# Kernel optimization log

Measured on AMD Instinct MI355X. Metric: run time of the kernel, lower is better.

Reference implementation:

```python
import jax, jax.numpy as jnp
import numpy as np

N_NODES = 100000


def gcn_conv(x, edge_index, W, b):
    # PyG GCNConv: add self-loops, symmetric normalization D^-1/2 (A+I) D^-1/2, then linear.
    n = x.shape[0]
    loop = jnp.arange(n, dtype=edge_index.dtype)
    src = jnp.concatenate([edge_index[0], loop])
    dst = jnp.concatenate([edge_index[1], loop])
    deg = jax.ops.segment_sum(jnp.ones_like(dst, dtype=x.dtype), dst, num_segments=n)
    dinv = jnp.where(deg > 0, jax.lax.rsqrt(deg), 0.0)
    norm = dinv[src] * dinv[dst]                      # [E+N]
    h = x @ W                                          # [N, out]
    msg = h[src] * norm[:, None]                       # gather + scale
    out = jax.ops.segment_sum(msg, dst, num_segments=n)  # scatter-add
    return out + b


def forward_one(x, edge_index, W1, b1, W2, b2, fc_w, fc_b):
    x = jax.nn.relu(gcn_conv(x, edge_index, W1, b1))
    x = jax.nn.relu(gcn_conv(x, edge_index, W2, b2))
    x = jnp.mean(x, axis=0)                            # [hidden]
    return x @ fc_w.T + fc_b


def setup_inputs() -> dict:
    key = jax.random.key(0)
    ks = jax.random.split(key, 10)
    d_in, d_h = 64, 64
    E = 1600000
    s = 1.0 / np.sqrt(d_in)
    return {
        "x1": jax.random.normal(ks[0], (N_NODES, d_in), jnp.float32),
        "x2": jax.random.normal(ks[1], (N_NODES, d_in), jnp.float32),
        "edge_index1": jax.random.randint(ks[2], (2, E), 0, N_NODES, jnp.int32),
        "edge_index2": jax.random.randint(ks[3], (2, E), 0, N_NODES, jnp.int32),
        "W1": jax.random.normal(ks[4], (d_in, d_h), jnp.float32) * s,
        "b1": jnp.zeros((d_h,), jnp.float32),
        "W2": jax.random.normal(ks[5], (d_h, d_h), jnp.float32) * s,
        "b2": jnp.zeros((d_h,), jnp.float32),
        "fc_w": jax.random.normal(ks[6], (d_h, d_h), jnp.float32) * s,
        "fc_b": jnp.zeros((d_h,), jnp.float32),
    }


def reference(x1, x2, edge_index1, edge_index2, W1, b1, W2, b2, fc_w, fc_b):
    out1 = forward_one(x1, edge_index1, W1, b1, W2, b2, fc_w, fc_b)
    out2 = forward_one(x2, edge_index2, W1, b1, W2, b2, fc_w, fc_b)
    return (out1, out2)
```

## Files before the change

kernel.cpp:

```cpp
#include <hip/hip_runtime.h>


#define TPB    256
#define CHUNK  128
#define SHIFT  7
#define KMAX   1024
#define CAP    2560
#define EPB    8192
#define CPAD   16

typedef __attribute__((ext_vector_type(8))) short short8;
typedef __attribute__((ext_vector_type(4))) float f32x4;
typedef __attribute__((ext_vector_type(2))) float float2v;

struct Ctx {
    const float* X; const int* esrc; const int* edst;
    unsigned int* temp; unsigned char* Hs2; unsigned char* Hs;
    unsigned int* csr; int* row_ptr; int* degA; float* dinv; int* cursorG;
    float* P; float* P2; float* outp;
};

__device__ __forceinline__ unsigned short f2bf(float x) {
    union { float f; unsigned int i; } c; c.f = x;
    unsigned int r = c.i + 0x7FFFu + ((c.i >> 16) & 1u);
    return (unsigned short)(r >> 16);
}
__device__ __forceinline__ unsigned char f2fp8(float x) {
    int p = __builtin_amdgcn_cvt_pk_fp8_f32(x, x, 0, false);
    return (unsigned char)(p & 0xFF);
}
__device__ __forceinline__ float2v up8lo(unsigned int w) {
    return __builtin_amdgcn_cvt_pk_f32_fp8(w, false);
}
__device__ __forceinline__ float2v up8hi(unsigned int w) {
    return __builtin_amdgcn_cvt_pk_f32_fp8(w, true);
}

__global__ void k_prepW2(const float* __restrict__ W1, const float* __restrict__ W2,
                         unsigned short* __restrict__ Wt1, unsigned short* __restrict__ Wt2) {
    const float* W = blockIdx.x ? W2 : W1;
    unsigned short* Wt = blockIdx.x ? Wt2 : Wt1;
    for (int i = threadIdx.x; i < 64 * 64; i += 256) {
        int n = i >> 6, k = i & 63;
        Wt[i] = f2bf(W[k * 64 + n]);
    }
}

__global__ void k_zeroCur(Ctx c0, Ctx c1, int nb0, int K, int N) {
    int b = blockIdx.x; Ctx c = c0;
    if (b >= nb0) { c = c1; b -= nb0; }
    int i = b * blockDim.x + threadIdx.x;
    if (i < K) c.cursorG[i * CPAD] = 0;
    if (b == 0 && threadIdx.x < 64) c.Hs[(size_t)N * 64 + threadIdx.x] = 0;
}

__global__ __launch_bounds__(1024) void k_binA(Ctx c0, Ctx c1, int nb0, int E, int K) {
    __shared__ int cnt[KMAX];
    __shared__ int ofs[KMAX];
    __shared__ int segBase[KMAX];
    __shared__ unsigned int sorted[EPB];
    __shared__ unsigned short bkt[EPB];
    int b = blockIdx.x; Ctx c = c0;
    if (b >= nb0) { c = c1; b -= nb0; }
    int tid = threadIdx.x;
    cnt[tid] = 0;
    __syncthreads();
    int base = b * EPB;
    int tot = E - base; if (tot > EPB) tot = EPB;
#pragma unroll
    for (int k = 0; k < EPB / 1024; ++k) {
        int e = base + k * 1024 + tid;
        if (e < E) atomicAdd(&cnt[c.edst[e] >> SHIFT], 1);
    }
    __syncthreads();
    int v = cnt[tid];
    segBase[tid] = v;
    __syncthreads();
#pragma unroll
    for (int off = 1; off < 1024; off <<= 1) {
        int t = (tid >= off) ? segBase[tid - off] : 0;
        __syncthreads();
        segBase[tid] += t;
        __syncthreads();
    }
    ofs[tid] = segBase[tid] - v;
    __syncthreads();
    if (tid < K) {
        segBase[tid] = v ? atomicAdd(&c.cursorG[tid * CPAD], v) : 0;
    } else {
        segBase[tid] = 0;
    }
    cnt[tid] = 0;
    __syncthreads();
#pragma unroll
    for (int k = 0; k < EPB / 1024; ++k) {
        int e = base + k * 1024 + tid;
        if (e < E) {
            int d = c.edst[e];
            int bk = d >> SHIFT;
            int r = atomicAdd(&cnt[bk], 1);
            int p = ofs[bk] + r;
            sorted[p] = ((unsigned int)(d & (CHUNK - 1)) << 17) | (unsigned int)c.esrc[e];
            bkt[p] = (unsigned short)bk;
        }
    }
    __syncthreads();
    for (int p = tid; p < tot; p += 1024) {
        unsigned int vv = sorted[p];
        int bk = bkt[p];
        int pos = segBase[bk] + (p - ofs[bk]);
        if (pos < CAP) c.temp[(size_t)bk * CAP + pos] = vv;
    }
}

__global__ __launch_bounds__(256) void k_csrb(Ctx c0, Ctx c1, int nb0, int N) {
    __shared__ int deg[CHUNK];
    __shared__ int lofs[CHUNK];
    __shared__ int cur[CHUNK];
    int b = blockIdx.x; Ctx c = c0;
    if (b >= nb0) { c = c1; b -= nb0; }
    int tid = threadIdx.x;
    if (tid < CHUNK) deg[tid] = 0;
    __syncthreads();
    int cnt = c.cursorG[b * CPAD]; if (cnt > CAP) cnt = CAP;
    const size_t tb = (size_t)b * CAP;
    for (int i = tid; i < cnt; i += 256) atomicAdd(&deg[c.temp[tb + i] >> 17], 1);
    __syncthreads();
    if (tid < CHUNK) lofs[tid] = deg[tid];
    __syncthreads();
#pragma unroll
    for (int off = 1; off < CHUNK; off <<= 1) {
        int t = (tid < CHUNK && tid >= off) ? lofs[tid - off] : 0;
        __syncthreads();
        if (tid < CHUNK) lofs[tid] += t;
        __syncthreads();
    }
    int base = b * CAP;
    if (tid < CHUNK) {
        int excl = lofs[tid] - deg[tid];
        lofs[tid] = excl;
        cur[tid] = 0;
        int node = b * CHUNK + tid;
        if (node < N) {
            c.row_ptr[node] = base + excl;
            c.degA[node] = deg[tid];
            c.dinv[node] = rsqrtf((float)deg[tid] + 1.0f);
        }
    }
    __syncthreads();
    for (int i = tid; i < cnt; i += 256) {
        unsigned int p = c.temp[tb + i];
        int dl = p >> 17;
        int rank = atomicAdd(&cur[dl], 1);
        c.csr[base + lofs[dl] + rank] = (p & 0x1FFFFu) << 6;
    }
}

__device__ __forceinline__ void mfma_tail(short8 a0, short8 a1,
                                          const unsigned short* __restrict__ Wt,
                                          unsigned char* __restrict__ Hs,
                                          int row0, int r, int q, int N) {
    short8 bfrag[4][2];
#pragma unroll
    for (int ct = 0; ct < 4; ++ct)
#pragma unroll
        for (int kb = 0; kb < 2; ++kb)
            bfrag[ct][kb] = *(const short8*)(Wt + (ct * 16 + r) * 64 + q * 8 + 32 * kb);
    f32x4 acc[4];
#pragma unroll
    for (int ct = 0; ct < 4; ++ct) {
        acc[ct] = (f32x4){0.0f, 0.0f, 0.0f, 0.0f};
        acc[ct] = __builtin_amdgcn_mfma_f32_16x16x32_bf16(a0, bfrag[ct][0], acc[ct], 0, 0, 0);
        acc[ct] = __builtin_amdgcn_mfma_f32_16x16x32_bf16(a1, bfrag[ct][1], acc[ct], 0, 0, 0);
    }
#pragma unroll
    for (int reg = 0; reg < 4; ++reg) {
        int row = row0 + q * 4 + reg;
        if (row < N) {
            size_t base = (size_t)row * 64 + r;
#pragma unroll
            for (int ct = 0; ct < 4; ++ct)
                Hs[base + ct * 16] = f2fp8(acc[ct][reg]);
        }
    }
}

__global__ __launch_bounds__(256) void k_gemm1(Ctx c0, Ctx c1, int nb0,
                                               const unsigned short* __restrict__ Wt,
                                               int nTiles, int N) {
    int b = blockIdx.x; Ctx c = c0;
    if (b >= nb0) { c = c1; b -= nb0; }
    int wave = threadIdx.x >> 6, lane = threadIdx.x & 63;
    int tile = b * 4 + wave;
    if (tile >= nTiles) return;
    int r = lane & 15, q = lane >> 4;
    int row0 = tile * 16;
    int row = row0 + r;
    int rr = row < N ? row : N - 1;
    float d = c.dinv[rr];
    const float* xrow = c.X + (size_t)rr * 64 + q * 8;
    short8 a0, a1;
#pragma unroll
    for (int j = 0; j < 8; ++j) a0[j] = (short)f2bf(xrow[j] * d);
#pragma unroll
    for (int j = 0; j < 8; ++j) a1[j] = (short)f2bf(xrow[32 + j] * d);
    mfma_tail(a0, a1, Wt, c.Hs, row0, r, q, N);
}

__device__ __forceinline__ void agg_map(int bi, int nb0, int swz,
                                        const Ctx& c0, const Ctx& c1,
                                        Ctx& c, int& b) {
    if (swz) {
        int graph = (bi >> 2) & 1;
        b = ((bi >> 3) << 2) | (bi & 3);
        c = graph ? c1 : c0;
    } else {
        b = bi; c = c0;
        if (b >= nb0) { c = c1; b -= nb0; }
    }
}

__device__ __forceinline__ void agg_issue8(const unsigned char* __restrict__ Hs,
                                           unsigned int idx, int slotbase, int lim,
                                           int hbase, int g, unsigned int s4,
                                           unsigned int* h) {
#pragma unroll
    for (int u = 0; u < 8; ++u) {
        if (slotbase + 2 * u >= lim) break;
        unsigned int su = (unsigned int)__shfl((int)idx, hbase + slotbase + 2 * u + g, 64);
        h[u] = *(const unsigned int*)(Hs + (su | s4));
    }
}
__device__ __forceinline__ void agg_cons8(const unsigned int* h, int slotbase, int lim,
                                          float2v* acc) {
#pragma unroll
    for (int u = 0; u < 8; ++u) {
        if (slotbase + 2 * u >= lim) break;
        acc[0] += up8lo(h[u]); acc[1] += up8hi(h[u]);
    }
}

__device__ __forceinline__ void agg_pair2(const unsigned char* __restrict__ Hs,
                                          const unsigned int* __restrict__ csr,
                                          int beg0, int deg0, int maxs0,
                                          int beg1, int deg1, int maxs1,
                                          int lane, unsigned int sent,
                                          float2v* acc0, float2v* acc1) {
    int hbase = lane & 32;
    int hl = lane & 31;
    int g = (lane >> 4) & 1;
    unsigned int s4 = (unsigned int)((lane & 15) * 4);
    unsigned int idx0 = (hl < deg0) ? csr[beg0 + hl] : sent;
    unsigned int idx1 = (hl < deg1) ? csr[beg1 + hl] : sent;
    int lim0 = maxs0 > 32 ? 32 : maxs0;
    int lim1 = maxs1 > 32 ? 32 : maxs1;
    unsigned int h0[8], h1[8];
    agg_issue8(Hs, idx0, 0, lim0, hbase, g, s4, h0);
    agg_issue8(Hs, idx1, 0, lim1, hbase, g, s4, h1);
    agg_cons8(h0, 0, lim0, acc0);
    if (lim0 > 16) agg_issue8(Hs, idx0, 16, lim0, hbase, g, s4, h0);
    agg_cons8(h1, 0, lim1, acc1);
    if (lim1 > 16) agg_issue8(Hs, idx1, 16, lim1, hbase, g, s4, h1);
    if (lim0 > 16) agg_cons8(h0, 16, lim0, acc0);
    if (lim1 > 16) agg_cons8(h1, 16, lim1, acc1);
    for (int base = 32; base < maxs0; base += 32) {
        unsigned int idx = (base + hl < deg0) ? csr[beg0 + base + hl] : sent;
        int lim = maxs0 - base; if (lim > 32) lim = 32;
        unsigned int hh[8];
        agg_issue8(Hs, idx, 0, lim, hbase, g, s4, hh);
        agg_cons8(hh, 0, lim, acc0);
        if (lim > 16) {
            agg_issue8(Hs, idx, 16, lim, hbase, g, s4, hh);
            agg_cons8(hh, 16, lim, acc0);
        }
    }
    for (int base = 32; base < maxs1; base += 32) {
        unsigned int idx = (base + hl < deg1) ? csr[beg1 + base + hl] : sent;
        int lim = maxs1 - base; if (lim > 32) lim = 32;
        unsigned int hh[8];
        agg_issue8(Hs, idx, 0, lim, hbase, g, s4, hh);
        agg_cons8(hh, 0, lim, acc1);
        if (lim > 16) {
            agg_issue8(Hs, idx, 16, lim, hbase, g, s4, hh);
            agg_cons8(hh, 16, lim, acc1);
        }
    }
#pragma unroll
    for (int k = 0; k < 2; ++k) {
        float2v o;
        o.x = __shfl_xor(acc0[k].x, 16, 64); o.y = __shfl_xor(acc0[k].y, 16, 64);
        acc0[k] += o;
        o.x = __shfl_xor(acc1[k].x, 16, 64); o.y = __shfl_xor(acc1[k].y, 16, 64);
        acc1[k] += o;
    }
}

__global__ __launch_bounds__(256) void k_agg1(Ctx c0, Ctx c1, int nb0, int swz,
                                              const float* __restrict__ bias,
                                              const unsigned short* __restrict__ Wt2,
                                              int n) {
    __shared__ unsigned short As[16][64];
    Ctx c; int b;
    agg_map(blockIdx.x, nb0, swz, c0, c1, c, b);
    int wave = threadIdx.x >> 6, lane = threadIdx.x & 63;
    int h = lane >> 5;
    int nbase = b * 16 + wave * 4;
    int node0 = nbase + h;
    int node1 = nbase + 2 + h;
    int nd0 = node0 < n ? node0 : 0;
    int nd1 = node1 < n ? node1 : 0;
    int beg0 = c.row_ptr[nd0];
    int beg1 = c.row_ptr[nd1];
    int deg0 = (node0 < n) ? c.degA[nd0] : 0;
    int deg1 = (node1 < n) ? c.degA[nd1] : 0;
    int od0 = __shfl_xor(deg0, 32, 64); int m0 = deg0 > od0 ? deg0 : od0;
    int od1 = __shfl_xor(deg1, 32, 64); int m1 = deg1 > od1 ? deg1 : od1;
    int maxs0 = __builtin_amdgcn_readfirstlane(m0);
    int maxs1 = __builtin_amdgcn_readfirstlane(m1);
    if (b == 0 && threadIdx.x < 64) c.Hs2[(size_t)n * 64 + threadIdx.x] = 0;
    float2v acc0[2] = {{0.f, 0.f}, {0.f, 0.f}};
    float2v acc1[2] = {{0.f, 0.f}, {0.f, 0.f}};
    agg_pair2(c.Hs, c.csr, beg0, deg0, maxs0, beg1, deg1, maxs1,
              lane, (unsigned int)n << 6, acc0, acc1);
    if (((lane >> 4) & 1) == 0) {
        int s = lane & 15;
#pragma unroll
        for (int pr = 0; pr < 2; ++pr) {
            const float2v* ac = pr ? acc1 : acc0;
            int node = nbase + pr * 2 + h;
            ushort4 o = {0, 0, 0, 0};
            if (node < n) {
                unsigned int hv = *(const unsigned int*)(c.Hs + (size_t)node * 64 + s * 4);
                float2v h0 = up8lo(hv), h1 = up8hi(hv);
                float4 bb = *(const float4*)(bias + s * 4);
                float d = c.dinv[node];
                o.x = f2bf(fmaxf(bb.x + d * (ac[0].x + h0.x), 0.0f) * d);
                o.y = f2bf(fmaxf(bb.y + d * (ac[0].y + h0.y), 0.0f) * d);
                o.z = f2bf(fmaxf(bb.z + d * (ac[1].x + h1.x), 0.0f) * d);
                o.w = f2bf(fmaxf(bb.w + d * (ac[1].y + h1.y), 0.0f) * d);
            }
            int row = wave * 4 + pr * 2 + h;
            *(ushort4*)(&As[row][(s * 4) ^ ((row & 7) << 3)]) = o;
        }
    }
    __syncthreads();
    {
        int r = lane & 15, q = lane >> 4;
        int sw = (r & 7) << 3;
        short8 a0 = *(const short8*)(&As[r][(q * 8) ^ sw]);
        short8 a1 = *(const short8*)(&As[r][(q * 8 + 32) ^ sw]);
        const unsigned short* wp = Wt2 + (wave * 16 + r) * 64 + q * 8;
        short8 b0 = *(const short8*)(wp);
        short8 b1 = *(const short8*)(wp + 32);
        f32x4 acc2 = {0.0f, 0.0f, 0.0f, 0.0f};
        acc2 = __builtin_amdgcn_mfma_f32_16x16x32_bf16(a0, b0, acc2, 0, 0, 0);
        acc2 = __builtin_amdgcn_mfma_f32_16x16x32_bf16(a1, b1, acc2, 0, 0, 0);
#pragma unroll
        for (int reg = 0; reg < 4; ++reg) {
            int l = q * 4 + reg;
            int row = b * 16 + l;
            if (row < n)
                c.Hs2[(size_t)row * 64 + wave * 16 + r] = f2fp8(acc2[reg]);
        }
    }
}

__global__ __launch_bounds__(256) void k_agg2(Ctx c0, Ctx c1, int nb0, int swz,
                                              const float* __restrict__ bias, int n) {
    __shared__ float red[16 * 64];
    Ctx c; int b;
    agg_map(blockIdx.x, nb0, swz, c0, c1, c, b);
    int wave = threadIdx.x >> 6, lane = threadIdx.x & 63;
    int h = lane >> 5;
    int nbase = b * 16 + wave * 4;
    int node0 = nbase + h;
    int node1 = nbase + 2 + h;
    int nd0 = node0 < n ? node0 : 0;
    int nd1 = node1 < n ? node1 : 0;
    int beg0 = c.row_ptr[nd0];
    int beg1 = c.row_ptr[nd1];
    int deg0 = (node0 < n) ? c.degA[nd0] : 0;
    int deg1 = (node1 < n) ? c.degA[nd1] : 0;
    int od0 = __shfl_xor(deg0, 32, 64); int m0 = deg0 > od0 ? deg0 : od0;
    int od1 = __shfl_xor(deg1, 32, 64); int m1 = deg1 > od1 ? deg1 : od1;
    int maxs0 = __builtin_amdgcn_readfirstlane(m0);
    int maxs1 = __builtin_amdgcn_readfirstlane(m1);
    float2v acc0[2] = {{0.f, 0.f}, {0.f, 0.f}};
    float2v acc1[2] = {{0.f, 0.f}, {0.f, 0.f}};
    agg_pair2(c.Hs2, c.csr, beg0, deg0, maxs0, beg1, deg1, maxs1,
              lane, (unsigned int)n << 6, acc0, acc1);
    if (((lane >> 4) & 1) == 0) {
        int s = lane & 15;
#pragma unroll
        for (int pr = 0; pr < 2; ++pr) {
            const float2v* ac = pr ? acc1 : acc0;
            int node = nbase + pr * 2 + h;
            float4 v = {0.f, 0.f, 0.f, 0.f};
            if (node < n) {
                unsigned int hv = *(const unsigned int*)(c.Hs2 + (size_t)node * 64 + s * 4);
                float2v h0 = up8lo(hv), h1 = up8hi(hv);
                float4 bb = *(const float4*)(bias + s * 4);
                float d = c.dinv[node];
                v.x = fmaxf(bb.x + d * (ac[0].x + h0.x), 0.0f);
                v.y = fmaxf(bb.y + d * (ac[0].y + h0.y), 0.0f);
                v.z = fmaxf(bb.z + d * (ac[1].x + h1.x), 0.0f);
                v.w = fmaxf(bb.w + d * (ac[1].y + h1.y), 0.0f);
            }
            *(float4*)(&red[(wave * 4 + pr * 2 + h) * 64 + s * 4]) = v;
        }
    }
    __syncthreads();
    if (threadIdx.x < 64) {
        float acc16 = 0.0f;
#pragma unroll
        for (int r = 0; r < 16; ++r) acc16 += red[r * 64 + threadIdx.x];
        c.P[(size_t)b * 64 + threadIdx.x] = acc16;
    }
}

__global__ void k_colsum(Ctx c0, Ctx c1, int nb0, int rows) {
    int b = blockIdx.x; Ctx c = c0;
    if (b >= nb0) { c = c1; b -= nb0; }
    int f = threadIdx.x;
    float acc = 0.0f;
    for (int r = b; r < rows; r += nb0) acc += c.P[(size_t)r * 64 + f];
    c.P2[b * 64 + f] = acc;
}

__global__ void k_fc(Ctx c0, Ctx c1, const float* __restrict__ fcw,
                     const float* __restrict__ fcb, int n) {
    Ctx c = blockIdx.x ? c1 : c0;
    __shared__ float S[64];
    int j = threadIdx.x;
    float s = 0.0f;
    for (int r = 0; r < 256; ++r) s += c.P2[r * 64 + j];
    S[j] = s;
    __syncthreads();
    float inv = 1.0f / (float)n;
    float acc = fcb[j];
#pragma unroll
    for (int k = 0; k < 64; ++k) acc += (S[k] * inv) * fcw[j * 64 + k];
    c.outp[j] = acc;
}

extern "C" void kernel_launch(void* const* d_in, const int* in_sizes, int n_in,
                              void* d_out, int out_size, void* d_ws, size_t ws_size,
                              hipStream_t stream) {
    const float* x[2]  = {(const float*)d_in[0], (const float*)d_in[1]};
    const int*   ei[2] = {(const int*)d_in[2], (const int*)d_in[3]};
    const float* W1  = (const float*)d_in[4];
    const float* b1  = (const float*)d_in[5];
    const float* W2  = (const float*)d_in[6];
    const float* b2  = (const float*)d_in[7];
    const float* fcw = (const float*)d_in[8];
    const float* fcb = (const float*)d_in[9];
    float* out = (float*)d_out;

    const int N  = in_sizes[0] / 64;
    const int E  = in_sizes[2] / 2;
    const int NF = N * 64;
    const int K  = (N + CHUNK - 1) / CHUNK;
    const int gGm  = (N + 15) / 16;
    const int gGmP = (gGm + 3) & ~3;
    const int nTiles = (N + 15) / 16;
    const int gMf = (nTiles + 3) / 4;
    const int gBin = (E + EPB - 1) / EPB;
    const int gK  = (K + TPB - 1) / TPB;

    auto al = [](size_t x) { return (x + 127) & ~(size_t)127; };
    size_t tempB = (size_t)K * CAP * 4;
    size_t hs2B  = (size_t)NF + 64;
    size_t szRegion = al(tempB > hs2B ? tempB : hs2B);
    size_t szHs  = al((size_t)NF + 64);
    size_t szCsr = al((size_t)K * CAP * 4);
    size_t szRp  = al((size_t)N * 4);
    size_t szDeg = al((size_t)N * 4);
    size_t szDi  = al((size_t)N * 4);
    size_t szCu  = al((size_t)K * CPAD * 4);
    size_t szP   = al((size_t)gGmP * 64 * 4);
    size_t szP2  = al((size_t)256 * 64 * 4);
    size_t setB  = szRegion + szHs + szCsr + szRp + szDeg + szDi + szCu + szP + szP2;
    size_t wtB   = 2 * al(64 * 64 * 2);
    bool batched = ws_size >= wtB + 2 * setB;

    char* base = (char*)d_ws;
    unsigned short* Wt1 = (unsigned short*)base;
    unsigned short* Wt2 = (unsigned short*)(base + al(64 * 64 * 2));

    auto mkctx = [&](int g, char* p) {
        Ctx c;
        c.X = x[g]; c.esrc = ei[g]; c.edst = ei[g] + E;
        c.temp = (unsigned int*)p; c.Hs2 = (unsigned char*)p; p += szRegion;
        c.Hs = (unsigned char*)p; p += szHs;
        c.csr = (unsigned int*)p; p += szCsr;
        c.row_ptr = (int*)p; p += szRp;
        c.degA = (int*)p; p += szDeg;
        c.dinv = (float*)p; p += szDi;
        c.cursorG = (int*)p; p += szCu;
        c.P = (float*)p; p += szP;
        c.P2 = (float*)p;
        c.outp = out + g * 64;
        return c;
    };
    char* set0 = base + wtB;
    Ctx c0 = mkctx(0, set0);
    Ctx c1 = mkctx(1, batched ? set0 + setB : set0);

    k_prepW2<<<2, 256, 0, stream>>>(W1, W2, Wt1, Wt2);

    auto pipe = [&](Ctx A, Ctx B, int mult) {
        int swz = (mult == 2) ? 1 : 0;
        k_zeroCur<<<mult * gK, TPB, 0, stream>>>(A, B, gK, K, N);
        k_binA<<<mult * gBin, 1024, 0, stream>>>(A, B, gBin, E, K);
        k_csrb<<<mult * K, 256, 0, stream>>>(A, B, K, N);
        k_gemm1<<<mult * gMf, 256, 0, stream>>>(A, B, gMf, Wt1, nTiles, N);
        k_agg1<<<mult * gGmP, 256, 0, stream>>>(A, B, gGmP, swz, b1, Wt2, N);
        k_agg2<<<mult * gGmP, 256, 0, stream>>>(A, B, gGmP, swz, b2, N);
        k_colsum<<<mult * 256, 64, 0, stream>>>(A, B, 256, gGmP);
        k_fc<<<mult, 64, 0, stream>>>(A, B, fcw, fcb, N);
    };

    if (batched) {
        pipe(c0, c1, 2);
    } else {
        pipe(c0, c0, 1);
        pipe(c1, c1, 1);
    }
}
```

Baseline: 285.4 us.

## Widen aggregation gathers to 8-byte loads and use wave-shuffle scans

Each lane in the neighbor aggregation now gathers 8 fp8 features per load instead of 4, so a half-wave processes four neighbors per step in place of two. This removes the second issue/consume round for degrees up to 32, at the cost of twice as many accumulator registers and an extra xor-shuffle reduction stage. The shared-memory Hillis-Steele prefix scans in the binning and CSR kernels are replaced with wavefront shuffle scans plus a small cross-wave fixup, which removes most of the barriers. The aggregation kernels also gain a minimum-blocks launch bound of 8.

```diff
diff --git a/kernel.cpp b/kernel.cpp
--- a/kernel.cpp
+++ b/kernel.cpp
@@ -12,6 +12,7 @@
 typedef __attribute__((ext_vector_type(8))) short short8;
 typedef __attribute__((ext_vector_type(4))) float f32x4;
 typedef __attribute__((ext_vector_type(2))) float float2v;
+typedef __attribute__((ext_vector_type(2))) unsigned int uint2v;
 
 struct Ctx {
     const float* X; const int* esrc; const int* edst;
@@ -58,6 +59,7 @@
     __shared__ int cnt[KMAX];
     __shared__ int ofs[KMAX];
     __shared__ int segBase[KMAX];
+    __shared__ int wsum[16];
     __shared__ unsigned int sorted[EPB];
     __shared__ unsigned short bkt[EPB];
     int b = blockIdx.x; Ctx c = c0;
@@ -74,17 +76,27 @@
     }
     __syncthreads();
     int v = cnt[tid];
-    segBase[tid] = v;
-    __syncthreads();
-#pragma unroll
-    for (int off = 1; off < 1024; off <<= 1) {
-        int t = (tid >= off) ? segBase[tid - off] : 0;
-        __syncthreads();
-        segBase[tid] += t;
-        __syncthreads();
-    }
-    ofs[tid] = segBase[tid] - v;
-    __syncthreads();
+    int lane = tid & 63, w = tid >> 6;
+    int x = v;
+#pragma unroll
+    for (int off = 1; off < 64; off <<= 1) {
+        int t = __shfl_up(x, off, 64);
+        if (lane >= off) x += t;
+    }
+    if (lane == 63) wsum[w] = x;
+    __syncthreads();
+    if (tid < 16) {
+        int y = wsum[tid];
+#pragma unroll
+        for (int off = 1; off < 16; off <<= 1) {
+            int t = __shfl_up(y, off, 16);
+            if ((tid & 15) >= off) y += t;
+        }
+        wsum[tid] = y;
+    }
+    __syncthreads();
+    int pre = w ? wsum[w - 1] : 0;
+    ofs[tid] = x + pre - v;
     if (tid < K) {
         segBase[tid] = v ? atomicAdd(&c.cursorG[tid * CPAD], v) : 0;
     } else {
@@ -117,6 +129,7 @@
     __shared__ int deg[CHUNK];
     __shared__ int lofs[CHUNK];
     __shared__ int cur[CHUNK];
+    __shared__ int wsum2[2];
     int b = blockIdx.x; Ctx c = c0;
     if (b >= nb0) { c = c1; b -= nb0; }
     int tid = threadIdx.x;
@@ -126,25 +139,26 @@
     const size_t tb = (size_t)b * CAP;
     for (int i = tid; i < cnt; i += 256) atomicAdd(&deg[c.temp[tb + i] >> 17], 1);
     __syncthreads();
-    if (tid < CHUNK) lofs[tid] = deg[tid];
-    __syncthreads();
-#pragma unroll
-    for (int off = 1; off < CHUNK; off <<= 1) {
-        int t = (tid < CHUNK && tid >= off) ? lofs[tid - off] : 0;
-        __syncthreads();
-        if (tid < CHUNK) lofs[tid] += t;
-        __syncthreads();
-    }
+    int vdeg = 0, x = 0;
+    if (tid < CHUNK) { vdeg = deg[tid]; x = vdeg; }
+#pragma unroll
+    for (int off = 1; off < 64; off <<= 1) {
+        int t = __shfl_up(x, off, 64);
+        if ((tid & 63) >= off) x += t;
+    }
+    if (tid < CHUNK && (tid & 63) == 63) wsum2[tid >> 6] = x;
+    __syncthreads();
     int base = b * CAP;
     if (tid < CHUNK) {
-        int excl = lofs[tid] - deg[tid];
+        int pre = (tid >> 6) ? wsum2[0] : 0;
+        int excl = x + pre - vdeg;
         lofs[tid] = excl;
         cur[tid] = 0;
         int node = b * CHUNK + tid;
         if (node < N) {
             c.row_ptr[node] = base + excl;
-            c.degA[node] = deg[tid];
-            c.dinv[node] = rsqrtf((float)deg[tid] + 1.0f);
+            c.degA[node] = vdeg;
+            c.dinv[node] = rsqrtf((float)vdeg + 1.0f);
         }
     }
     __syncthreads();
@@ -220,23 +234,23 @@
     }
 }
 
-__device__ __forceinline__ void agg_issue8(const unsigned char* __restrict__ Hs,
-                                           unsigned int idx, int slotbase, int lim,
-                                           int hbase, int g, unsigned int s4,
-                                           unsigned int* h) {
+__device__ __forceinline__ void agg_issue8w(const unsigned char* __restrict__ Hs,
+                                            unsigned int idx, int lim,
+                                            int hbase, int j, unsigned int s8,
+                                            uint2v* h) {
 #pragma unroll
     for (int u = 0; u < 8; ++u) {
-        if (slotbase + 2 * u >= lim) break;
-        unsigned int su = (unsigned int)__shfl((int)idx, hbase + slotbase + 2 * u + g, 64);
-        h[u] = *(const unsigned int*)(Hs + (su | s4));
-    }
-}
-__device__ __forceinline__ void agg_cons8(const unsigned int* h, int slotbase, int lim,
-                                          float2v* acc) {
+        if (4 * u >= lim) break;
+        unsigned int su = (unsigned int)__shfl((int)idx, hbase + 4 * u + j, 64);
+        h[u] = *(const uint2v*)(Hs + (su | s8));
+    }
+}
+__device__ __forceinline__ void agg_cons8w(const uint2v* h, int lim, float2v* acc) {
 #pragma unroll
     for (int u = 0; u < 8; ++u) {
-        if (slotbase + 2 * u >= lim) break;
-        acc[0] += up8lo(h[u]); acc[1] += up8hi(h[u]);
+        if (4 * u >= lim) break;
+        acc[0] += up8lo(h[u][0]); acc[1] += up8hi(h[u][0]);
+        acc[2] += up8lo(h[u][1]); acc[3] += up8hi(h[u][1]);
     }
 }
 
@@ -248,57 +262,49 @@
                                           float2v* acc0, float2v* acc1) {
     int hbase = lane & 32;
     int hl = lane & 31;
-    int g = (lane >> 4) & 1;
-    unsigned int s4 = (unsigned int)((lane & 15) * 4);
+    int j = (hl >> 3) & 3;
+    unsigned int s8 = (unsigned int)((lane & 7) * 8);
     unsigned int idx0 = (hl < deg0) ? csr[beg0 + hl] : sent;
     unsigned int idx1 = (hl < deg1) ? csr[beg1 + hl] : sent;
     int lim0 = maxs0 > 32 ? 32 : maxs0;
     int lim1 = maxs1 > 32 ? 32 : maxs1;
-    unsigned int h0[8], h1[8];
-    agg_issue8(Hs, idx0, 0, lim0, hbase, g, s4, h0);
-    agg_issue8(Hs, idx1, 0, lim1, hbase, g, s4, h1);
-    agg_cons8(h0, 0, lim0, acc0);
-    if (lim0 > 16) agg_issue8(Hs, idx0, 16, lim0, hbase, g, s4, h0);
-    agg_cons8(h1, 0, lim1, acc1);
-    if (lim1 > 16) agg_issue8(Hs, idx1, 16, lim1, hbase, g, s4, h1);
-    if (lim0 > 16) agg_cons8(h0, 16, lim0, acc0);
-    if (lim1 > 16) agg_cons8(h1, 16, lim1, acc1);
+    uint2v h0[8], h1[8];
+    agg_issue8w(Hs, idx0, lim0, hbase, j, s8, h0);
+    agg_issue8w(Hs, idx1, lim1, hbase, j, s8, h1);
+    agg_cons8w(h0, lim0, acc0);
+    agg_cons8w(h1, lim1, acc1);
     for (int base = 32; base < maxs0; base += 32) {
         unsigned int idx = (base + hl < deg0) ? csr[beg0 + base + hl] : sent;
         int lim = maxs0 - base; if (lim > 32) lim = 32;
-        unsigned int hh[8];
-        agg_issue8(Hs, idx, 0, lim, hbase, g, s4, hh);
-        agg_cons8(hh, 0, lim, acc0);
-        if (lim > 16) {
-            agg_issue8(Hs, idx, 16, lim, hbase, g, s4, hh);
-            agg_cons8(hh, 16, lim, acc0);
-        }
+        uint2v hh[8];
+        agg_issue8w(Hs, idx, lim, hbase, j, s8, hh);
+        agg_cons8w(hh, lim, acc0);
     }
     for (int base = 32; base < maxs1; base += 32) {
         unsigned int idx = (base + hl < deg1) ? csr[beg1 + base + hl] : sent;
         int lim = maxs1 - base; if (lim > 32) lim = 32;
-        unsigned int hh[8];
-        agg_issue8(Hs, idx, 0, lim, hbase, g, s4, hh);
-        agg_cons8(hh, 0, lim, acc1);
-        if (lim > 16) {
-            agg_issue8(Hs, idx, 16, lim, hbase, g, s4, hh);
-            agg_cons8(hh, 16, lim, acc1);
-        }
-    }
-#pragma unroll
-    for (int k = 0; k < 2; ++k) {
+        uint2v hh[8];
+        agg_issue8w(Hs, idx, lim, hbase, j, s8, hh);
+        agg_cons8w(hh, lim, acc1);
+    }
+#pragma unroll
+    for (int k = 0; k < 4; ++k) {
         float2v o;
+        o.x = __shfl_xor(acc0[k].x, 8, 64);  o.y = __shfl_xor(acc0[k].y, 8, 64);
+        acc0[k] += o;
         o.x = __shfl_xor(acc0[k].x, 16, 64); o.y = __shfl_xor(acc0[k].y, 16, 64);
         acc0[k] += o;
+        o.x = __shfl_xor(acc1[k].x, 8, 64);  o.y = __shfl_xor(acc1[k].y, 8, 64);
+        acc1[k] += o;
         o.x = __shfl_xor(acc1[k].x, 16, 64); o.y = __shfl_xor(acc1[k].y, 16, 64);
         acc1[k] += o;
     }
 }
 
-__global__ __launch_bounds__(256) void k_agg1(Ctx c0, Ctx c1, int nb0, int swz,
-                                              const float* __restrict__ bias,
-                                              const unsigned short* __restrict__ Wt2,
-                                              int n) {
+__global__ __launch_bounds__(256, 8) void k_agg1(Ctx c0, Ctx c1, int nb0, int swz,
+                                                 const float* __restrict__ bias,
+                                                 const unsigned short* __restrict__ Wt2,
+                                                 int n) {
     __shared__ unsigned short As[16][64];
     Ctx c; int b;
     agg_map(blockIdx.x, nb0, swz, c0, c1, c, b);
@@ -318,29 +324,37 @@
     int maxs0 = __builtin_amdgcn_readfirstlane(m0);
     int maxs1 = __builtin_amdgcn_readfirstlane(m1);
     if (b == 0 && threadIdx.x < 64) c.Hs2[(size_t)n * 64 + threadIdx.x] = 0;
-    float2v acc0[2] = {{0.f, 0.f}, {0.f, 0.f}};
-    float2v acc1[2] = {{0.f, 0.f}, {0.f, 0.f}};
+    float2v acc0[4] = {{0.f,0.f},{0.f,0.f},{0.f,0.f},{0.f,0.f}};
+    float2v acc1[4] = {{0.f,0.f},{0.f,0.f},{0.f,0.f},{0.f,0.f}};
     agg_pair2(c.Hs, c.csr, beg0, deg0, maxs0, beg1, deg1, maxs1,
               lane, (unsigned int)n << 6, acc0, acc1);
-    if (((lane >> 4) & 1) == 0) {
-        int s = lane & 15;
+    if (((lane >> 3) & 3) == 0) {
+        int s = lane & 7;
 #pragma unroll
         for (int pr = 0; pr < 2; ++pr) {
             const float2v* ac = pr ? acc1 : acc0;
             int node = nbase + pr * 2 + h;
-            ushort4 o = {0, 0, 0, 0};
+            ushort4 oA = {0, 0, 0, 0}, oB = {0, 0, 0, 0};
             if (node < n) {
-                unsigned int hv = *(const unsigned int*)(c.Hs + (size_t)node * 64 + s * 4);
-                float2v h0 = up8lo(hv), h1 = up8hi(hv);
-                float4 bb = *(const float4*)(bias + s * 4);
+                uint2v hv = *(const uint2v*)(c.Hs + (size_t)node * 64 + s * 8);
+                float2v h0 = up8lo(hv[0]), h1 = up8hi(hv[0]);
+                float2v h2 = up8lo(hv[1]), h3 = up8hi(hv[1]);
+                float4 ba = *(const float4*)(bias + s * 8);
+                float4 bb = *(const float4*)(bias + s * 8 + 4);
                 float d = c.dinv[node];
-                o.x = f2bf(fmaxf(bb.x + d * (ac[0].x + h0.x), 0.0f) * d);
-                o.y = f2bf(fmaxf(bb.y + d * (ac[0].y + h0.y), 0.0f) * d);
-                o.z = f2bf(fmaxf(bb.z + d * (ac[1].x + h1.x), 0.0f) * d);
-                o.w = f2bf(fmaxf(bb.w + d * (ac[1].y + h1.y), 0.0f) * d);
+                oA.x = f2bf(fmaxf(ba.x + d * (ac[0].x + h0.x), 0.0f) * d);
+                oA.y = f2bf(fmaxf(ba.y + d * (ac[0].y + h0.y), 0.0f) * d);
+                oA.z = f2bf(fmaxf(ba.z + d * (ac[1].x + h1.x), 0.0f) * d);
+                oA.w = f2bf(fmaxf(ba.w + d * (ac[1].y + h1.y), 0.0f) * d);
+                oB.x = f2bf(fmaxf(bb.x + d * (ac[2].x + h2.x), 0.0f) * d);
+                oB.y = f2bf(fmaxf(bb.y + d * (ac[2].y + h2.y), 0.0f) * d);
+                oB.z = f2bf(fmaxf(bb.z + d * (ac[3].x + h3.x), 0.0f) * d);
+                oB.w = f2bf(fmaxf(bb.w + d * (ac[3].y + h3.y), 0.0f) * d);
             }
             int row = wave * 4 + pr * 2 + h;
-            *(ushort4*)(&As[row][(s * 4) ^ ((row & 7) << 3)]) = o;
+            int col = (s * 8) ^ ((row & 7) << 3);
+            *(ushort4*)(&As[row][col]) = oA;
+            *(ushort4*)(&As[row][col + 4]) = oB;
         }
     }
     __syncthreads();
@@ -365,8 +379,8 @@
     }
 }
 
-__global__ __launch_bounds__(256) void k_agg2(Ctx c0, Ctx c1, int nb0, int swz,
-                                              const float* __restrict__ bias, int n) {
+__global__ __launch_bounds__(256, 8) void k_agg2(Ctx c0, Ctx c1, int nb0, int swz,
+                                                 const float* __restrict__ bias, int n) {
     __shared__ float red[16 * 64];
     Ctx c; int b;
     agg_map(blockIdx.x, nb0, swz, c0, c1, c, b);
@@ -385,28 +399,36 @@
     int od1 = __shfl_xor(deg1, 32, 64); int m1 = deg1 > od1 ? deg1 : od1;
     int maxs0 = __builtin_amdgcn_readfirstlane(m0);
     int maxs1 = __builtin_amdgcn_readfirstlane(m1);
-    float2v acc0[2] = {{0.f, 0.f}, {0.f, 0.f}};
-    float2v acc1[2] = {{0.f, 0.f}, {0.f, 0.f}};
+    float2v acc0[4] = {{0.f,0.f},{0.f,0.f},{0.f,0.f},{0.f,0.f}};
+    float2v acc1[4] = {{0.f,0.f},{0.f,0.f},{0.f,0.f},{0.f,0.f}};
     agg_pair2(c.Hs2, c.csr, beg0, deg0, maxs0, beg1, deg1, maxs1,
               lane, (unsigned int)n << 6, acc0, acc1);
-    if (((lane >> 4) & 1) == 0) {
-        int s = lane & 15;
+    if (((lane >> 3) & 3) == 0) {
+        int s = lane & 7;
 #pragma unroll
         for (int pr = 0; pr < 2; ++pr) {
             const float2v* ac = pr ? acc1 : acc0;
             int node = nbase + pr * 2 + h;
-            float4 v = {0.f, 0.f, 0.f, 0.f};
+            float4 vA = {0.f, 0.f, 0.f, 0.f}, vB = {0.f, 0.f, 0.f, 0.f};
             if (node < n) {
-                unsigned int hv = *(const unsigned int*)(c.Hs2 + (size_t)node * 64 + s * 4);
-                float2v h0 = up8lo(hv), h1 = up8hi(hv);
-                float4 bb = *(const float4*)(bias + s * 4);
+                uint2v hv = *(const uint2v*)(c.Hs2 + (size_t)node * 64 + s * 8);
+                float2v h0 = up8lo(hv[0]), h1 = up8hi(hv[0]);
+                float2v h2 = up8lo(hv[1]), h3 = up8hi(hv[1]);
+                float4 ba = *(const float4*)(bias + s * 8);
+                float4 bb = *(const float4*)(bias + s * 8 + 4);
                 float d = c.dinv[node];
-                v.x = fmaxf(bb.x + d * (ac[0].x + h0.x), 0.0f);
-                v.y = fmaxf(bb.y + d * (ac[0].y + h0.y), 0.0f);
-                v.z = fmaxf(bb.z + d * (ac[1].x + h1.x), 0.0f);
-                v.w = fmaxf(bb.w + d * (ac[1].y + h1.y), 0.0f);
+                vA.x = fmaxf(ba.x + d * (ac[0].x + h0.x), 0.0f);
+                vA.y = fmaxf(ba.y + d * (ac[0].y + h0.y), 0.0f);
+                vA.z = fmaxf(ba.z + d * (ac[1].x + h1.x), 0.0f);
+                vA.w = fmaxf(ba.w + d * (ac[1].y + h1.y), 0.0f);
+                vB.x = fmaxf(bb.x + d * (ac[2].x + h2.x), 0.0f);
+                vB.y = fmaxf(bb.y + d * (ac[2].y + h2.y), 0.0f);
+                vB.z = fmaxf(bb.z + d * (ac[3].x + h3.x), 0.0f);
+                vB.w = fmaxf(bb.w + d * (ac[3].y + h3.y), 0.0f);
             }
-            *(float4*)(&red[(wave * 4 + pr * 2 + h) * 64 + s * 4]) = v;
+            int row = wave * 4 + pr * 2 + h;
+            *(float4*)(&red[row * 64 + s * 8]) = vA;
+            *(float4*)(&red[row * 64 + s * 8 + 4]) = vB;
         }
     }
     __syncthreads();
```

Measured after the change: 280.7 us. Within noise of the previous version (-1.7%).
